# Performance work log

Measured on AMD Instinct MI355X. Metric: run time of the kernel, lower is better.

## Reference

```python
import jax, jax.numpy as jnp
import numpy as np

GAMMA = 2.0
EPS = 1e-12  # tf.nn.l2_normalize epsilon


def setup_inputs() -> dict:
    key = jax.random.key(0)
    k1, k2 = jax.random.split(key)
    B, H, W_, C = 8, 56, 56, 256
    x = jax.random.normal(k1, (B, H, W_, C), dtype=jnp.float32)
    W = jax.random.normal(k2, (C, C), dtype=jnp.float32) * 0.05
    return {"x": x, "W": W}


def reference(x, W):
    B, H, Wd, C = x.shape
    hw = H * Wd
    # transform branch: 1x1 conv, no bias (num_layers=1)
    t = jnp.einsum('bhwc,cd->bhwd', x, W).reshape(B, hw, C)
    # pixel affinity: cosine similarity (tf: -cosine_similarity == cos sim)
    xf = x.reshape(B, hw, C)
    inv_norm = jax.lax.rsqrt(jnp.maximum(jnp.sum(xf * xf, axis=-1, keepdims=True), EPS))
    xn = xf * inv_norm
    sim = jnp.einsum('bic,bjc->bij', xn, xn)  # [B, hw, hw]
    sim = jnp.power(jax.nn.relu(sim), GAMMA)
    y = jnp.einsum('bij,bjc->bic', sim, t)
    return y.reshape(B, H, Wd, C)
```

## Files before the change

### kernel.cpp

```cpp
#include <hip/hip_runtime.h>

#define HW 3136
#define CH 256
#define NJT 49
#define NPIX 25088

typedef __attribute__((ext_vector_type(8))) short bf16x8;
typedef __attribute__((ext_vector_type(4))) float f32x4;
typedef unsigned short u16;
typedef unsigned int u32;

static __device__ __forceinline__ u16 f2bf(float f){
  union { float f; u32 u; } v; v.f = f;
  u32 r = v.u + 0x7FFFu + ((v.u >> 16) & 1u);
  return (u16)(r >> 16);
}

static __device__ __forceinline__ void gload16(const void* g, void* l){
  __builtin_amdgcn_global_load_lds(
      (const __attribute__((address_space(1))) unsigned int*)g,
      (__attribute__((address_space(3))) unsigned int*)l, 16, 0, 0);
}

__global__ __launch_bounds__(256) void prep_norm(const float* __restrict__ x,
                                                 u16* __restrict__ x_bf,
                                                 u16* __restrict__ xn_bf){
  const int row  = blockIdx.x * 4 + (threadIdx.x >> 6);
  const int lane = threadIdx.x & 63;
  const float4 v = *(const float4*)(x + (size_t)row * CH + lane * 4);
  float ss = v.x*v.x + v.y*v.y + v.z*v.z + v.w*v.w;
  #pragma unroll
  for (int off = 32; off; off >>= 1) ss += __shfl_xor(ss, off);
  const float inv = rsqrtf(fmaxf(ss, 1e-12f));
  ushort4 xb, nb;
  xb.x = f2bf(v.x);     xb.y = f2bf(v.y);     xb.z = f2bf(v.z);     xb.w = f2bf(v.w);
  nb.x = f2bf(v.x*inv); nb.y = f2bf(v.y*inv); nb.z = f2bf(v.z*inv); nb.w = f2bf(v.w*inv);
  *(ushort4*)(x_bf  + (size_t)row*CH + lane*4) = xb;
  *(ushort4*)(xn_bf + (size_t)row*CH + lane*4) = nb;
}

__global__ __launch_bounds__(256) void prep_wt(const float* __restrict__ W,
                                               u16* __restrict__ Wt){
  const int o = blockIdx.x, i = threadIdx.x;
  Wt[o*CH + i] = f2bf(W[i*CH + o]);
}

__global__ __launch_bounds__(256) void gemm_t(const u16* __restrict__ x_bf,
                                              const u16* __restrict__ Wt,
                                              u16* __restrict__ tT){
  __shared__ u16 sT[256*64];
  const int jt = blockIdx.x, b = blockIdx.y;
  const int tid = threadIdx.x, wid = tid >> 6, lane = tid & 63;
  const int l15 = lane & 15, l4 = lane >> 4;
  const int j0 = jt * 64;
  const int jrow = j0 + wid*16 + l15;
  const u16* ap = x_bf + ((size_t)b*HW + jrow)*CH + l4*8;

  f32x4 acc[16];
  #pragma unroll
  for (int n = 0; n < 16; ++n) acc[n] = f32x4{0.f,0.f,0.f,0.f};

  #pragma unroll
  for (int ks = 0; ks < 8; ++ks){
    const bf16x8 a = *(const bf16x8*)(ap + ks*32);
    #pragma unroll
    for (int n0 = 0; n0 < 16; ++n0){
      const bf16x8 bb = *(const bf16x8*)(Wt + (n0*16 + l15)*CH + ks*32 + l4*8);
      acc[n0] = __builtin_amdgcn_mfma_f32_16x16x32_bf16(a, bb, acc[n0], 0, 0, 0);
    }
  }
  #pragma unroll
  for (int n0 = 0; n0 < 16; ++n0){
    const int c = n0*16 + l15;
    const int jloc = wid*16 + l4*4;
    const int gj = jloc >> 3;
    ushort4 w4;
    w4.x = f2bf(acc[n0][0]); w4.y = f2bf(acc[n0][1]);
    w4.z = f2bf(acc[n0][2]); w4.w = f2bf(acc[n0][3]);
    *(ushort4*)&sT[c*64 + ((gj ^ (c & 7)) * 8) + (jloc & 7)] = w4;
  }
  __syncthreads();
  #pragma unroll
  for (int p = 0; p < 8; ++p){
    const int c = p*32 + (tid >> 3);
    const int q = tid & 7;
    const bf16x8 v = *(const bf16x8*)&sT[c*64 + ((q ^ (c & 7)) * 8)];
    *(bf16x8*)(tT + ((size_t)b*CH + c)*HW + j0 + q*8) = v;
  }
}

__global__ __launch_bounds__(256, 2) void ppm_main(const u16* __restrict__ xn,
                                                   const u16* __restrict__ tT,
                                                   float* __restrict__ out){
  __shared__ u16 sXJ[64*256];
  __shared__ u16 sTJ[256*64];
  __shared__ u16 sS [64*64];

  const int it = blockIdx.x, b = blockIdx.y;
  const int tid = threadIdx.x, wid = tid >> 6, lane = tid & 63;
  const int l15 = lane & 15, l4 = lane >> 4;
  const int i0 = it * 64;
  const int wqj = wid >> 1, wqi = wid & 1;

  bf16x8 aq[2][8];
  #pragma unroll
  for (int nb = 0; nb < 2; ++nb){
    const u16* p = xn + ((size_t)b*HW + i0 + wqi*32 + nb*16 + l15)*CH + l4*8;
    #pragma unroll
    for (int kb = 0; kb < 8; ++kb) aq[nb][kb] = *(const bf16x8*)(p + kb*32);
  }

  f32x4 accY[4][4];
  #pragma unroll
  for (int mb = 0; mb < 4; ++mb)
    #pragma unroll
    for (int nb = 0; nb < 4; ++nb) accY[mb][nb] = f32x4{0.f,0.f,0.f,0.f};

  const int sx_rl = lane >> 5, sx_sc = lane & 31;
  const int st_cl = lane >> 3, st_sc = lane & 7;

  for (int jt = 0; jt < NJT; ++jt){
    const int j0 = jt * 64;
    #pragma unroll
    for (int q = 0; q < 8; ++q){
      const int m = wid*8 + q;
      { const int row = 2*m + sx_rl;
        const int g = sx_sc ^ (row & 7);
        gload16(xn + ((size_t)b*HW + j0 + row)*CH + g*8, &sXJ[m*512]); }
      { const int c = 8*m + st_cl;
        const int g = st_sc ^ (c & 7);
        gload16(tT + ((size_t)b*CH + c)*HW + j0 + g*8, &sTJ[m*512]); }
    }
    __syncthreads();

    f32x4 accS[2][2];
    #pragma unroll
    for (int mb = 0; mb < 2; ++mb)
      #pragma unroll
      for (int nb = 0; nb < 2; ++nb) accS[mb][nb] = f32x4{0.f,0.f,0.f,0.f};
    #pragma unroll
    for (int kb = 0; kb < 8; ++kb){
      bf16x8 a[2];
      #pragma unroll
      for (int mb = 0; mb < 2; ++mb){
        const int rj = wqj*32 + mb*16 + l15;
        const int gk = kb*4 + l4;
        a[mb] = *(const bf16x8*)&sXJ[rj*256 + ((gk ^ (rj & 7)) * 8)];
      }
      #pragma unroll
      for (int mb = 0; mb < 2; ++mb)
        #pragma unroll
        for (int nb = 0; nb < 2; ++nb)
          accS[mb][nb] = __builtin_amdgcn_mfma_f32_16x16x32_bf16(a[mb], aq[nb][kb], accS[mb][nb], 0, 0, 0);
    }
    #pragma unroll
    for (int mb = 0; mb < 2; ++mb)
      #pragma unroll
      for (int nb = 0; nb < 2; ++nb){
        const int i_loc = wqi*32 + nb*16 + l15;
        const int jloc  = wqj*32 + mb*16 + l4*4;
        const int gj = jloc >> 3;
        float v0 = fmaxf(accS[mb][nb][0], 0.f); v0 *= v0;
        float v1 = fmaxf(accS[mb][nb][1], 0.f); v1 *= v1;
        float v2 = fmaxf(accS[mb][nb][2], 0.f); v2 *= v2;
        float v3 = fmaxf(accS[mb][nb][3], 0.f); v3 *= v3;
        ushort4 w4; w4.x = f2bf(v0); w4.y = f2bf(v1); w4.z = f2bf(v2); w4.w = f2bf(v3);
        *(ushort4*)&sS[i_loc*64 + ((gj ^ (i_loc & 7)) * 8) + (jloc & 7)] = w4;
      }
    __syncthreads();

    #pragma unroll
    for (int kb = 0; kb < 2; ++kb){
      bf16x8 sA[4], sB[4];
      #pragma unroll
      for (int mb = 0; mb < 4; ++mb){
        const int i = mb*16 + l15;
        const int gj = kb*4 + l4;
        sA[mb] = *(const bf16x8*)&sS[i*64 + ((gj ^ (i & 7)) * 8)];
      }
      #pragma unroll
      for (int nb = 0; nb < 4; ++nb){
        const int c = wid*64 + nb*16 + l15;
        const int gj = kb*4 + l4;
        sB[nb] = *(const bf16x8*)&sTJ[c*64 + ((gj ^ (c & 7)) * 8)];
      }
      #pragma unroll
      for (int mb = 0; mb < 4; ++mb)
        #pragma unroll
        for (int nb = 0; nb < 4; ++nb)
          accY[mb][nb] = __builtin_amdgcn_mfma_f32_16x16x32_bf16(sA[mb], sB[nb], accY[mb][nb], 0, 0, 0);
    }
    __syncthreads();
  }

  #pragma unroll
  for (int mb = 0; mb < 4; ++mb)
    #pragma unroll
    for (int nb = 0; nb < 4; ++nb)
      #pragma unroll
      for (int r = 0; r < 4; ++r)
        out[((size_t)b*HW + i0 + mb*16 + l4*4 + r)*CH + wid*64 + nb*16 + l15] = accY[mb][nb][r];
}

extern "C" void kernel_launch(void* const* d_in, const int* in_sizes, int n_in,
                              void* d_out, int out_size, void* d_ws, size_t ws_size,
                              hipStream_t stream){
  const float* x = (const float*)d_in[0];
  const float* W = (const float*)d_in[1];
  float* out = (float*)d_out;
  char* ws = (char*)d_ws;

  const size_t SZ = (size_t)NPIX * CH * sizeof(u16);
  u16* x_bf  = (u16*)(ws);
  u16* xn_bf = (u16*)(ws + SZ);
  u16* tT    = (u16*)(ws + 2*SZ);
  u16* Wt    = (u16*)(ws + 3*SZ);

  prep_norm<<<NPIX/4, 256, 0, stream>>>(x, x_bf, xn_bf);
  prep_wt<<<CH, CH, 0, stream>>>(W, Wt);
  gemm_t<<<dim3(NJT, 8), 256, 0, stream>>>(x_bf, Wt, tT);
  ppm_main<<<dim3(NJT, 8), 256, 0, stream>>>(xn_bf, tT, out);
}
```

Baseline: 162.6 us.

## Fuse normalization into transform GEMM and retile main kernel with double buffering

Drops the separate prep_norm kernel: gemm_t now reads fp32 x directly, computes row norms with shuffles and writes xn_bf itself. The main kernel moves to 128-row i tiles with 512 threads, 32x32x16 MFMA, and double-buffered global-to-LDS staging of the j tiles so loads overlap compute. This removes one launch and a bf16 copy of x, and roughly halves reloads of the j tiles across blocks. In exchange it needs much more LDS per block (about 144 KB), which lowers occupancy, and the i dimension is padded, so the last tile does some wasted work.

```diff
diff --git a/kernel.cpp b/kernel.cpp
--- a/kernel.cpp
+++ b/kernel.cpp
@@ -3,10 +3,12 @@
 #define HW 3136
 #define CH 256
 #define NJT 49
+#define NIT 25
 #define NPIX 25088
 
 typedef __attribute__((ext_vector_type(8))) short bf16x8;
 typedef __attribute__((ext_vector_type(4))) float f32x4;
+typedef __attribute__((ext_vector_type(16))) float f32x16;
 typedef unsigned short u16;
 typedef unsigned int u32;
 
@@ -22,21 +24,15 @@
       (__attribute__((address_space(3))) unsigned int*)l, 16, 0, 0);
 }
 
-__global__ __launch_bounds__(256) void prep_norm(const float* __restrict__ x,
-                                                 u16* __restrict__ x_bf,
-                                                 u16* __restrict__ xn_bf){
-  const int row  = blockIdx.x * 4 + (threadIdx.x >> 6);
-  const int lane = threadIdx.x & 63;
-  const float4 v = *(const float4*)(x + (size_t)row * CH + lane * 4);
-  float ss = v.x*v.x + v.y*v.y + v.z*v.z + v.w*v.w;
-  #pragma unroll
-  for (int off = 32; off; off >>= 1) ss += __shfl_xor(ss, off);
-  const float inv = rsqrtf(fmaxf(ss, 1e-12f));
-  ushort4 xb, nb;
-  xb.x = f2bf(v.x);     xb.y = f2bf(v.y);     xb.z = f2bf(v.z);     xb.w = f2bf(v.w);
-  nb.x = f2bf(v.x*inv); nb.y = f2bf(v.y*inv); nb.z = f2bf(v.z*inv); nb.w = f2bf(v.w*inv);
-  *(ushort4*)(x_bf  + (size_t)row*CH + lane*4) = xb;
-  *(ushort4*)(xn_bf + (size_t)row*CH + lane*4) = nb;
+static __device__ __forceinline__ f32x16 zero16(){
+  f32x16 v;
+  #pragma unroll
+  for (int e = 0; e < 16; ++e) v[e] = 0.f;
+  return v;
+}
+
+static __device__ __forceinline__ int ssw(int i, int c){
+  return (((c + (i >> 3)) & 7) ^ (i & 7));
 }
 
 __global__ __launch_bounds__(256) void prep_wt(const float* __restrict__ W,
@@ -45,28 +41,55 @@
   Wt[o*CH + i] = f2bf(W[i*CH + o]);
 }
 
-__global__ __launch_bounds__(256) void gemm_t(const u16* __restrict__ x_bf,
+__global__ __launch_bounds__(256) void gemm_t(const float* __restrict__ x,
                                               const u16* __restrict__ Wt,
+                                              u16* __restrict__ xn_bf,
                                               u16* __restrict__ tT){
   __shared__ u16 sT[256*64];
   const int jt = blockIdx.x, b = blockIdx.y;
   const int tid = threadIdx.x, wid = tid >> 6, lane = tid & 63;
   const int l15 = lane & 15, l4 = lane >> 4;
   const int j0 = jt * 64;
-  const int jrow = j0 + wid*16 + l15;
-  const u16* ap = x_bf + ((size_t)b*HW + jrow)*CH + l4*8;
+  const int row = j0 + wid*16 + l15;
+  const float* xp = x + ((size_t)b*HW + row)*CH + l4*8;
+
+  float xv[8][8];
+  float ss = 0.f;
+  #pragma unroll
+  for (int kb = 0; kb < 8; ++kb){
+    const float4 v0 = *(const float4*)(xp + kb*32);
+    const float4 v1 = *(const float4*)(xp + kb*32 + 4);
+    xv[kb][0]=v0.x; xv[kb][1]=v0.y; xv[kb][2]=v0.z; xv[kb][3]=v0.w;
+    xv[kb][4]=v1.x; xv[kb][5]=v1.y; xv[kb][6]=v1.z; xv[kb][7]=v1.w;
+    #pragma unroll
+    for (int e = 0; e < 8; ++e) ss += xv[kb][e]*xv[kb][e];
+  }
+  ss += __shfl_xor(ss, 16);
+  ss += __shfl_xor(ss, 32);
+  const float inv = rsqrtf(fmaxf(ss, 1e-12f));
+
+  bf16x8 ax[8];
+  #pragma unroll
+  for (int kb = 0; kb < 8; ++kb){
+    bf16x8 a, n;
+    #pragma unroll
+    for (int e = 0; e < 8; ++e){
+      a[e] = (short)f2bf(xv[kb][e]);
+      n[e] = (short)f2bf(xv[kb][e]*inv);
+    }
+    ax[kb] = a;
+    *(bf16x8*)(xn_bf + ((size_t)b*HW + row)*CH + kb*32 + l4*8) = n;
+  }
 
   f32x4 acc[16];
   #pragma unroll
   for (int n = 0; n < 16; ++n) acc[n] = f32x4{0.f,0.f,0.f,0.f};
-
-  #pragma unroll
-  for (int ks = 0; ks < 8; ++ks){
-    const bf16x8 a = *(const bf16x8*)(ap + ks*32);
+  #pragma unroll
+  for (int kb = 0; kb < 8; ++kb){
     #pragma unroll
     for (int n0 = 0; n0 < 16; ++n0){
-      const bf16x8 bb = *(const bf16x8*)(Wt + (n0*16 + l15)*CH + ks*32 + l4*8);
-      acc[n0] = __builtin_amdgcn_mfma_f32_16x16x32_bf16(a, bb, acc[n0], 0, 0, 0);
+      const bf16x8 bb = *(const bf16x8*)(Wt + (n0*16 + l15)*CH + kb*32 + l4*8);
+      acc[n0] = __builtin_amdgcn_mfma_f32_16x16x32_bf16(ax[kb], bb, acc[n0], 0, 0, 0);
     }
   }
   #pragma unroll
@@ -89,117 +112,122 @@
   }
 }
 
-__global__ __launch_bounds__(256, 2) void ppm_main(const u16* __restrict__ xn,
-                                                   const u16* __restrict__ tT,
-                                                   float* __restrict__ out){
-  __shared__ u16 sXJ[64*256];
-  __shared__ u16 sTJ[256*64];
-  __shared__ u16 sS [64*64];
+__global__ __launch_bounds__(512) void ppm_main(const u16* __restrict__ xn,
+                                                const u16* __restrict__ tT,
+                                                float* __restrict__ out){
+  __shared__ u16 sXJ[2][64*256];
+  __shared__ u16 sTJ[2][256*64];
+  __shared__ u16 sS [128*64];
 
   const int it = blockIdx.x, b = blockIdx.y;
   const int tid = threadIdx.x, wid = tid >> 6, lane = tid & 63;
-  const int l15 = lane & 15, l4 = lane >> 4;
-  const int i0 = it * 64;
-  const int wqj = wid >> 1, wqi = wid & 1;
-
-  bf16x8 aq[2][8];
-  #pragma unroll
-  for (int nb = 0; nb < 2; ++nb){
-    const u16* p = xn + ((size_t)b*HW + i0 + wqi*32 + nb*16 + l15)*CH + l4*8;
-    #pragma unroll
-    for (int kb = 0; kb < 8; ++kb) aq[nb][kb] = *(const bf16x8*)(p + kb*32);
-  }
-
-  f32x4 accY[4][4];
-  #pragma unroll
-  for (int mb = 0; mb < 4; ++mb)
-    #pragma unroll
-    for (int nb = 0; nb < 4; ++nb) accY[mb][nb] = f32x4{0.f,0.f,0.f,0.f};
-
-  const int sx_rl = lane >> 5, sx_sc = lane & 31;
-  const int st_cl = lane >> 3, st_sc = lane & 7;
-
-  for (int jt = 0; jt < NJT; ++jt){
+  const int l31 = lane & 31, hi = lane >> 5;
+  const int i0 = it * 128;
+  const int wqj = wid >> 2, wqi = wid & 3;
+  const int wpi = wid >> 2, wpc = wid & 3;
+
+  bf16x8 aq[16];
+  {
+    int irow = i0 + wqi*32 + l31;
+    if (irow >= HW) irow = HW - 1;
+    const u16* p = xn + ((size_t)b*HW + irow)*CH + hi*8;
+    #pragma unroll
+    for (int kb = 0; kb < 16; ++kb) aq[kb] = *(const bf16x8*)(p + kb*16);
+  }
+
+  f32x16 accY[2][2];
+  #pragma unroll
+  for (int mi = 0; mi < 2; ++mi)
+    #pragma unroll
+    for (int ni = 0; ni < 2; ++ni) accY[mi][ni] = zero16();
+
+  const size_t xbase = (size_t)b*HW;
+  const size_t tbase = (size_t)b*CH;
+
+  auto STAGE = [&](int buf, int jt){
     const int j0 = jt * 64;
     #pragma unroll
-    for (int q = 0; q < 8; ++q){
-      const int m = wid*8 + q;
-      { const int row = 2*m + sx_rl;
-        const int g = sx_sc ^ (row & 7);
-        gload16(xn + ((size_t)b*HW + j0 + row)*CH + g*8, &sXJ[m*512]); }
-      { const int c = 8*m + st_cl;
-        const int g = st_sc ^ (c & 7);
-        gload16(tT + ((size_t)b*CH + c)*HW + j0 + g*8, &sTJ[m*512]); }
+    for (int q = 0; q < 4; ++q){
+      const int m = q*512 + tid;
+      { const int row = m >> 5, g = m & 31;
+        gload16(xn + (xbase + j0 + row)*CH + ((g ^ (row & 7)) * 8), &sXJ[buf][m*8]); }
+      { const int c = m >> 3, g = m & 7;
+        gload16(tT + (tbase + c)*HW + j0 + ((g ^ (c & 7)) * 8), &sTJ[buf][m*8]); }
+    }
+  };
+
+  auto ITER = [&](int buf, int jt, bool stg){
+    if (stg) STAGE(buf ^ 1, jt + 1);
+
+    f32x16 sa = zero16(), sb = zero16();
+    const int rj = wqj*32 + l31;
+    const int rsw = rj & 7;
+    #pragma unroll
+    for (int kb = 0; kb < 16; kb += 2){
+      const bf16x8 a0 = *(const bf16x8*)&sXJ[buf][rj*256 + (((kb*2 + hi)     ^ rsw) * 8)];
+      const bf16x8 a1 = *(const bf16x8*)&sXJ[buf][rj*256 + (((kb*2 + 2 + hi) ^ rsw) * 8)];
+      sa = __builtin_amdgcn_mfma_f32_32x32x16_bf16(a0, aq[kb],   sa, 0, 0, 0);
+      sb = __builtin_amdgcn_mfma_f32_32x32x16_bf16(a1, aq[kb+1], sb, 0, 0, 0);
+    }
+    const int i_loc = wqi*32 + l31;
+    #pragma unroll
+    for (int q = 0; q < 4; ++q){
+      ushort4 w4;
+      #pragma unroll
+      for (int r = 0; r < 4; ++r){
+        float v = sa[q*4 + r] + sb[q*4 + r];
+        v = fmaxf(v, 0.f);
+        v *= v;
+        ((u16*)&w4)[r] = f2bf(v);
+      }
+      const int jb = q*8 + hi*4;
+      const int jl = wqj*32 + jb;
+      *(ushort4*)&sS[i_loc*64 + ssw(i_loc, jl >> 3)*8 + (jb & 7)] = w4;
     }
     __syncthreads();
 
-    f32x4 accS[2][2];
-    #pragma unroll
-    for (int mb = 0; mb < 2; ++mb)
-      #pragma unroll
-      for (int nb = 0; nb < 2; ++nb) accS[mb][nb] = f32x4{0.f,0.f,0.f,0.f};
-    #pragma unroll
-    for (int kb = 0; kb < 8; ++kb){
-      bf16x8 a[2];
-      #pragma unroll
-      for (int mb = 0; mb < 2; ++mb){
-        const int rj = wqj*32 + mb*16 + l15;
-        const int gk = kb*4 + l4;
-        a[mb] = *(const bf16x8*)&sXJ[rj*256 + ((gk ^ (rj & 7)) * 8)];
-      }
-      #pragma unroll
-      for (int mb = 0; mb < 2; ++mb)
+    #pragma unroll
+    for (int kb = 0; kb < 4; ++kb){
+      bf16x8 pa[2], pb[2];
+      #pragma unroll
+      for (int mi = 0; mi < 2; ++mi){
+        const int i = wpi*64 + mi*32 + l31;
+        pa[mi] = *(const bf16x8*)&sS[i*64 + ssw(i, kb*2 + hi)*8];
+      }
+      #pragma unroll
+      for (int ni = 0; ni < 2; ++ni){
+        const int c = wpc*64 + ni*32 + l31;
+        pb[ni] = *(const bf16x8*)&sTJ[buf][c*64 + (((kb*2 + hi) ^ (c & 7)) * 8)];
+      }
+      #pragma unroll
+      for (int mi = 0; mi < 2; ++mi)
         #pragma unroll
-        for (int nb = 0; nb < 2; ++nb)
-          accS[mb][nb] = __builtin_amdgcn_mfma_f32_16x16x32_bf16(a[mb], aq[nb][kb], accS[mb][nb], 0, 0, 0);
-    }
-    #pragma unroll
-    for (int mb = 0; mb < 2; ++mb)
-      #pragma unroll
-      for (int nb = 0; nb < 2; ++nb){
-        const int i_loc = wqi*32 + nb*16 + l15;
-        const int jloc  = wqj*32 + mb*16 + l4*4;
-        const int gj = jloc >> 3;
-        float v0 = fmaxf(accS[mb][nb][0], 0.f); v0 *= v0;
-        float v1 = fmaxf(accS[mb][nb][1], 0.f); v1 *= v1;
-        float v2 = fmaxf(accS[mb][nb][2], 0.f); v2 *= v2;
-        float v3 = fmaxf(accS[mb][nb][3], 0.f); v3 *= v3;
-        ushort4 w4; w4.x = f2bf(v0); w4.y = f2bf(v1); w4.z = f2bf(v2); w4.w = f2bf(v3);
-        *(ushort4*)&sS[i_loc*64 + ((gj ^ (i_loc & 7)) * 8) + (jloc & 7)] = w4;
-      }
+        for (int ni = 0; ni < 2; ++ni)
+          accY[mi][ni] = __builtin_amdgcn_mfma_f32_32x32x16_bf16(pa[mi], pb[ni], accY[mi][ni], 0, 0, 0);
+    }
     __syncthreads();
-
-    #pragma unroll
-    for (int kb = 0; kb < 2; ++kb){
-      bf16x8 sA[4], sB[4];
-      #pragma unroll
-      for (int mb = 0; mb < 4; ++mb){
-        const int i = mb*16 + l15;
-        const int gj = kb*4 + l4;
-        sA[mb] = *(const bf16x8*)&sS[i*64 + ((gj ^ (i & 7)) * 8)];
-      }
-      #pragma unroll
-      for (int nb = 0; nb < 4; ++nb){
-        const int c = wid*64 + nb*16 + l15;
-        const int gj = kb*4 + l4;
-        sB[nb] = *(const bf16x8*)&sTJ[c*64 + ((gj ^ (c & 7)) * 8)];
-      }
-      #pragma unroll
-      for (int mb = 0; mb < 4; ++mb)
-        #pragma unroll
-        for (int nb = 0; nb < 4; ++nb)
-          accY[mb][nb] = __builtin_amdgcn_mfma_f32_16x16x32_bf16(sA[mb], sB[nb], accY[mb][nb], 0, 0, 0);
-    }
-    __syncthreads();
-  }
-
-  #pragma unroll
-  for (int mb = 0; mb < 4; ++mb)
-    #pragma unroll
-    for (int nb = 0; nb < 4; ++nb)
-      #pragma unroll
-      for (int r = 0; r < 4; ++r)
-        out[((size_t)b*HW + i0 + mb*16 + l4*4 + r)*CH + wid*64 + nb*16 + l15] = accY[mb][nb][r];
+  };
+
+  STAGE(0, 0);
+  __syncthreads();
+
+  #pragma unroll 1
+  for (int jt = 0; jt < NJT - 1; jt += 2){
+    ITER(0, jt,     true);
+    ITER(1, jt + 1, jt + 2 < NJT);
+  }
+  ITER(0, NJT - 1, false);
+
+  #pragma unroll
+  for (int mi = 0; mi < 2; ++mi)
+    #pragma unroll
+    for (int ni = 0; ni < 2; ++ni)
+      #pragma unroll
+      for (int r = 0; r < 16; ++r){
+        const int row = i0 + wpi*64 + mi*32 + (r & 3) + 8*(r >> 2) + 4*hi;
+        if (row < HW)
+          out[((size_t)b*HW + row)*CH + wpc*64 + ni*32 + l31] = accY[mi][ni][r];
+      }
 }
 
 extern "C" void kernel_launch(void* const* d_in, const int* in_sizes, int n_in,
@@ -211,13 +239,11 @@
   char* ws = (char*)d_ws;
 
   const size_t SZ = (size_t)NPIX * CH * sizeof(u16);
-  u16* x_bf  = (u16*)(ws);
-  u16* xn_bf = (u16*)(ws + SZ);
-  u16* tT    = (u16*)(ws + 2*SZ);
-  u16* Wt    = (u16*)(ws + 3*SZ);
-
-  prep_norm<<<NPIX/4, 256, 0, stream>>>(x, x_bf, xn_bf);
+  u16* xn_bf = (u16*)(ws);
+  u16* tT    = (u16*)(ws + SZ);
+  u16* Wt    = (u16*)(ws + 2*SZ);
+
   prep_wt<<<CH, CH, 0, stream>>>(W, Wt);
-  gemm_t<<<dim3(NJT, 8), 256, 0, stream>>>(x_bf, Wt, tT);
-  ppm_main<<<dim3(NJT, 8), 256, 0, stream>>>(xn_bf, tT, out);
-}
+  gemm_t<<<dim3(NJT, 8), 256, 0, stream>>>(x, Wt, xn_bf, tT);
+  ppm_main<<<dim3(NIT, 8), 512, 0, stream>>>(xn_bf, tT, out);
+}
```

New measurement: 156.5 us. -3.8%, faster.
